# Kernel tuning notes

Measured on AMD Instinct MI355X. Metric: run time of the kernel, lower is better.

Reference implementation:

```python
import jax, jax.numpy as jnp
import numpy as np

NUM_FREQS = 10
Z_SIZE = 256
HIDDEN = 256
N_LAYERS = 8
N_POLY = 100000
PE_DIM = 2 * NUM_FREQS + 2 * NUM_FREQS * 2 + 4  # 64
IN1 = PE_DIM + Z_SIZE        # 320
IN_MID = HIDDEN + IN1        # 576
SLOPE = 0.01


def setup_inputs() -> dict:
    key = jax.random.key(0)
    ks = jax.random.split(key, 12)
    B = 131072
    xy = jax.random.normal(ks[0], (B, 2), dtype=jnp.float32)
    idx = jax.random.randint(ks[1], (B,), 0, N_POLY, dtype=jnp.int64 if jax.config.jax_enable_x64 else jnp.int32)
    emb = jax.random.normal(ks[2], (N_POLY, Z_SIZE), dtype=jnp.float32) * 0.01
    s = 0.02
    W1a = jax.random.normal(ks[3], (IN1, HIDDEN), dtype=jnp.float32) * s
    b1a = jnp.zeros((HIDDEN,), jnp.float32)
    W1b = jax.random.normal(ks[4], (HIDDEN, HIDDEN), dtype=jnp.float32) * s
    b1b = jnp.zeros((HIDDEN,), jnp.float32)
    Wa = jax.random.normal(ks[5], (N_LAYERS, IN_MID, HIDDEN), dtype=jnp.float32) * s
    ba = jnp.zeros((N_LAYERS, HIDDEN), jnp.float32)
    Wb = jax.random.normal(ks[6], (N_LAYERS, HIDDEN, HIDDEN), dtype=jnp.float32) * s
    bb = jnp.zeros((N_LAYERS, HIDDEN), jnp.float32)
    W2 = jax.random.normal(ks[7], (HIDDEN, 1), dtype=jnp.float32) * s
    b2 = jnp.zeros((1,), jnp.float32)
    return {"xy": xy, "idx": idx, "emb": emb, "W1a": W1a, "b1a": b1a,
            "W1b": W1b, "b1b": b1b, "Wa": Wa, "ba": ba, "Wb": Wb, "bb": bb,
            "W2": W2, "b2": b2}


def _pos_encode(xy):
    # linspace freq bands (log_sampling=False default)
    freq = jnp.linspace(1.0, 6.0, NUM_FREQS).astype(xy.dtype)  # (F,)
    xf = xy[:, None, :] * freq[:, None]                         # (B,F,2)
    # cat([x_input, sin, cos], dim=1) then reshape -> (B, (1+2F)*2)
    out = jnp.concatenate([xy[:, None, :], jnp.sin(xf), jnp.cos(xf)], axis=1)
    out = out.reshape(xy.shape[0], -1)                          # (B,42)
    # polar fourier encoding
    r = jnp.sqrt(xy[:, 0] ** 2 + xy[:, 1] ** 2)                 # (B,)
    rf = r[:, None] * freq                                      # (B,F)
    pe = jnp.concatenate([xy, jnp.sin(rf), jnp.cos(rf)], axis=-1)  # (B,22)
    return jnp.concatenate([out, pe], axis=-1)                  # (B,64)


def reference(xy, idx, emb, W1a, b1a, W1b, b1b, Wa, ba, Wb, bb, W2, b2):
    feat = _pos_encode(xy)                       # (B,64)
    z = emb[idx]                                 # (B,256)
    xy_z = jnp.concatenate([feat, z], axis=1)    # (B,320)
    x = jax.nn.leaky_relu(xy_z @ W1a + b1a, SLOPE) @ W1b + b1b  # (B,256)
    for i in range(N_LAYERS):
        h = jnp.concatenate([xy_z, x], axis=1)   # (B,576)
        x = jax.nn.leaky_relu(h @ Wa[i] + ba[i], SLOPE) @ Wb[i] + bb[i]
    return x @ W2 + b2                           # (B,1)
```

## Files before the change

### kernel.cpp

```cpp
#include <hip/hip_runtime.h>
#include <hip/hip_bf16.h>


typedef __attribute__((ext_vector_type(8))) __bf16 bfv8;
typedef __attribute__((ext_vector_type(8))) short s16x8;
typedef __attribute__((ext_vector_type(4))) float f32x4;
typedef __attribute__((ext_vector_type(4))) int i32x4;

__device__ __forceinline__ short f2bf(float f) {
  unsigned u = __builtin_bit_cast(unsigned, f);
  u = (u + 0x7fffu + ((u >> 16) & 1u)) >> 16;
  return (short)u;
}
__device__ __forceinline__ float bf2f(short s) {
  unsigned u = ((unsigned)(unsigned short)s) << 16;
  return __builtin_bit_cast(float, u);
}
__device__ __forceinline__ int swzaddr(int base, int stride, int row, int colbyte) {
  return base + row * stride + (colbyte ^ (((row & 7) << 4) ^ ((row & 8) << 2)));
}
__device__ __forceinline__ void ldsbar() {
  __builtin_amdgcn_sched_barrier(0);
  asm volatile("s_waitcnt lgkmcnt(0)");
  __builtin_amdgcn_s_barrier();
  __builtin_amdgcn_sched_barrier(0);
}

__global__ void pack_weights_kernel(const float* __restrict__ W1a, const float* __restrict__ W1b,
                                    const float* __restrict__ Wa, const float* __restrict__ Wb,
                                    short* __restrict__ ws) {
  int p = blockIdx.x * blockDim.x + threadIdx.x;
  const int P1 = 10240;
  const int P2 = P1 + 8192;
  const int P3 = P2 + 8 * 18432;
  const int P4 = P3 + 8 * 8192;
  if (p >= P4) return;
  const float* src;
  int q;
  if (p < P1)      { src = W1a; q = p; }
  else if (p < P2) { src = W1b; q = p - P1; }
  else if (p < P3) { q = p - P2; int l = q / 18432; q -= l * 18432; src = Wa + l * 147456; }
  else             { q = p - P3; int l = q / 8192;  q -= l * 8192;  src = Wb + l * 65536; }
  const int lane = q & 63, t = q >> 6, nt = t & 15, kt = t >> 4;
  const int k0 = kt * 32 + ((lane >> 4) << 3);
  const int n  = ((nt >> 1) << 5) + ((lane & 15) << 1) + (nt & 1);
  short* dst = ws + (size_t)p * 8;
#pragma unroll
  for (int i = 0; i < 8; ++i) dst[i] = f2bf(src[(size_t)(k0 + i) * 256 + n]);
}

struct BPre { bfv8 b0, b1; };
struct AFrag { bfv8 r0, r1, r2, r3; };
struct Pre { BPre b; AFrag a; };

__device__ __forceinline__ bfv8 bfrag(const short* __restrict__ wp, int kt, int nt, int lane) {
  const short* base = wp + (((size_t)(kt * 16 + nt)) << 9);
  return *(const bfv8*)(base + (lane << 3));
}

template<int NKT, int SPLITKT, bool LEAKY, bool MIDBAR, bool PRE_A, bool PRE_NEXT_A>
__device__ __forceinline__ Pre do_gemm(short* lds,
    int a1Base, int a1S, int a2Base, int a2S,
    const short* __restrict__ wp, const short* __restrict__ wpn,
    const float* __restrict__ bias, int outBase,
    int wc, int lane, Pre pre)
{
  const int lo = lane & 15, hi = lane >> 4;
  const int ntb = wc << 1;
  const float2 bv = *(const float2*)(bias + (wc << 5) + (lo << 1));
  f32x4 acc[4][2];
#pragma unroll
  for (int r = 0; r < 4; ++r) { acc[r][0] = (f32x4)0.f; acc[r][1] = (f32x4)0.f; }

  const int xr  = ((lo & 7) << 4) ^ ((lo & 8) << 2);
  const int hib = hi << 4;
  const char* A1E = (const char*)lds + a1Base + lo * a1S + ((     hib) ^ xr);
  const char* A1O = (const char*)lds + a1Base + lo * a1S + ((64 + hib) ^ xr);
  const char* A2E = (const char*)lds + a2Base + lo * a2S + ((     hib) ^ xr);
  const char* A2O = (const char*)lds + a2Base + lo * a2S + ((64 + hib) ^ xr);

  auto aLoad = [&](int kt, AFrag& dst) {
    const bool g1 = kt < SPLITKT;
    const int kk  = g1 ? kt : kt - SPLITKT;
    const int st  = g1 ? a1S : a2S;
    const char* b = (g1 ? ((kk & 1) ? A1O : A1E) : ((kk & 1) ? A2O : A2E)) + (kk >> 1) * 128;
    dst.r0 = *(const bfv8*)(b);
    dst.r1 = *(const bfv8*)(b + (st << 4));
    dst.r2 = *(const bfv8*)(b + (st << 5));
    dst.r3 = *(const bfv8*)(b + (st << 4) * 3);
  };

  bfv8 bst[4][2];
  AFrag ast[3];
  bst[0][0] = pre.b.b0; bst[0][1] = pre.b.b1;
  if (NKT > 1) { bst[1][0] = bfrag(wp, 1, ntb, lane); bst[1][1] = bfrag(wp, 1, ntb + 1, lane); }
  if (NKT > 2) { bst[2][0] = bfrag(wp, 2, ntb, lane); bst[2][1] = bfrag(wp, 2, ntb + 1, lane); }
  if (PRE_A) ast[0] = pre.a; else aLoad(0, ast[0]);
  if (NKT > 1) aLoad(1, ast[1]);
  Pre nxt;

#pragma unroll
  for (int i = 0; i < NKT; ++i) {
    if (MIDBAR && i == SPLITKT - 2) ldsbar();
    if (i + 3 < NKT) {
      bst[(i + 3) & 3][0] = bfrag(wp, i + 3, ntb, lane);
      bst[(i + 3) & 3][1] = bfrag(wp, i + 3, ntb + 1, lane);
    } else if (i + 3 == NKT || (NKT <= 3 && i == 0)) {
      nxt.b.b0 = bfrag(wpn, 0, ntb, lane);
      nxt.b.b1 = bfrag(wpn, 0, ntb + 1, lane);
    }
    if (i + 2 < NKT) aLoad(i + 2, ast[(i + 2) % 3]);
    if (PRE_NEXT_A && i == NKT - 1) {
      const char* bx = (const char*)lds + lo * 640 + (hib ^ xr);
      nxt.a.r0 = *(const bfv8*)(bx);
      nxt.a.r1 = *(const bfv8*)(bx + 640 * 16);
      nxt.a.r2 = *(const bfv8*)(bx + 640 * 32);
      nxt.a.r3 = *(const bfv8*)(bx + 640 * 48);
    }
    const AFrag& ac = ast[i % 3];
    __builtin_amdgcn_s_setprio(1);
    acc[0][0] = __builtin_amdgcn_mfma_f32_16x16x32_bf16(ac.r0, bst[i & 3][0], acc[0][0], 0, 0, 0);
    acc[0][1] = __builtin_amdgcn_mfma_f32_16x16x32_bf16(ac.r0, bst[i & 3][1], acc[0][1], 0, 0, 0);
    acc[1][0] = __builtin_amdgcn_mfma_f32_16x16x32_bf16(ac.r1, bst[i & 3][0], acc[1][0], 0, 0, 0);
    acc[1][1] = __builtin_amdgcn_mfma_f32_16x16x32_bf16(ac.r1, bst[i & 3][1], acc[1][1], 0, 0, 0);
    acc[2][0] = __builtin_amdgcn_mfma_f32_16x16x32_bf16(ac.r2, bst[i & 3][0], acc[2][0], 0, 0, 0);
    acc[2][1] = __builtin_amdgcn_mfma_f32_16x16x32_bf16(ac.r2, bst[i & 3][1], acc[2][1], 0, 0, 0);
    acc[3][0] = __builtin_amdgcn_mfma_f32_16x16x32_bf16(ac.r3, bst[i & 3][0], acc[3][0], 0, 0, 0);
    acc[3][1] = __builtin_amdgcn_mfma_f32_16x16x32_bf16(ac.r3, bst[i & 3][1], acc[3][1], 0, 0, 0);
    __builtin_amdgcn_s_setprio(0);
  }
#pragma unroll
  for (int rt = 0; rt < 4; ++rt)
#pragma unroll
    for (int rr = 0; rr < 4; ++rr) {
      float v0 = acc[rt][0][rr] + bv.x;
      float v1 = acc[rt][1][rr] + bv.y;
      if (LEAKY) { v0 = fmaxf(v0, 0.01f * v0); v1 = fmaxf(v1, 0.01f * v1); }
      unsigned pk;
      asm("v_cvt_pk_bf16_f32 %0, %1, %2" : "=v"(pk) : "v"(v0), "v"(v1));
      const int orow = (rt << 4) + (hi << 2) + rr;
      *(unsigned*)((char*)lds + swzaddr(outBase, 512, orow, (wc << 6) + (lo << 2))) = pk;
    }
  return nxt;
}

__launch_bounds__(512, 1)
__global__ void geo2vec_kernel(const float* __restrict__ xy, const int* __restrict__ idx,
    const float* __restrict__ emb,
    const float* __restrict__ b1a, const float* __restrict__ b1b,
    const float* __restrict__ ba, const float* __restrict__ bb,
    const float* __restrict__ W2, const float* __restrict__ b2,
    const short* __restrict__ wp, float* __restrict__ out)
{
  __shared__ short lds[53248];
  const int tid = threadIdx.x;
  const int lane = tid & 63;
  const int wc = __builtin_amdgcn_readfirstlane(tid >> 6);

  Pre pre;
  pre.b.b0 = bfrag(wp, 0, (wc << 1), lane);
  pre.b.b1 = bfrag(wp, 0, (wc << 1) + 1, lane);

  {
    const int g = tid >> 3, j = tid & 7;
    const int row = blockIdx.x * 64 + g;
    const float xv = xy[2 * row], yv = xy[2 * row + 1];
    const float rv = sqrtf(xv * xv + yv * yv);
    union { short s[8]; i32x4 v; } tmp;
#pragma unroll
    for (int i = 0; i < 8; ++i) {
      const int c = 8 * j + i;
      float fv;
      if (c < 2)       fv = c ? yv : xv;
      else if (c < 22) { int m = c - 2;  float f = 1.0f + (5.0f / 9.0f) * (m >> 1); fv = sinf(((m & 1) ? yv : xv) * f); }
      else if (c < 42) { int m = c - 22; float f = 1.0f + (5.0f / 9.0f) * (m >> 1); fv = cosf(((m & 1) ? yv : xv) * f); }
      else if (c < 44) fv = (c == 42) ? xv : yv;
      else if (c < 54) fv = sinf(rv * (1.0f + (5.0f / 9.0f) * (c - 44)));
      else             fv = cosf(rv * (1.0f + (5.0f / 9.0f) * (c - 54)));
      tmp.s[i] = f2bf(fv);
    }
    *(i32x4*)((char*)lds + swzaddr(0, 640, g, j << 4)) = tmp.v;
    const float* zr = emb + (size_t)(unsigned)idx[row] * 256;
#pragma unroll
    for (int c4 = 0; c4 < 4; ++c4) {
      const int cel = j * 32 + c4 * 8;
      const float4 f0 = *(const float4*)(zr + cel);
      const float4 f1 = *(const float4*)(zr + cel + 4);
      union { short s[8]; i32x4 v; } t2;
      t2.s[0] = f2bf(f0.x); t2.s[1] = f2bf(f0.y); t2.s[2] = f2bf(f0.z); t2.s[3] = f2bf(f0.w);
      t2.s[4] = f2bf(f1.x); t2.s[5] = f2bf(f1.y); t2.s[6] = f2bf(f1.z); t2.s[7] = f2bf(f1.w);
      *(i32x4*)((char*)lds + swzaddr(0, 640, g, (64 + cel) << 1)) = t2.v;
    }
  }
  ldsbar();

  pre = do_gemm<10, 10, true,  false, false, false>(lds, 0, 640, 0, 640,
        wp, wp + 81920, b1a, 73728, wc, lane, pre);
  ldsbar();
  pre = do_gemm<8, 8, false, false, false, true>(lds, 73728, 512, 73728, 512,
        wp + 81920, wp + 147456, b1b, 40960, wc, lane, pre);
  for (int l = 0; l < 8; ++l) {
    const short* wa = wp + 147456 + l * 147456;
    const short* wb = wp + 1327104 + l * 65536;
    const short* wan = (l < 7) ? (wa + 147456) : wp;
    pre = do_gemm<18, 10, true, true, true, false>(lds, 0, 640, 40960, 512,
          wa, wb, ba + l * 256, 73728, wc, lane, pre);
    ldsbar();
    pre = do_gemm<8, 8, false, false, false, true>(lds, 73728, 512, 73728, 512,
          wb, wan, bb + l * 256, 40960, wc, lane, pre);
  }
  ldsbar();

  {
    const int r = tid >> 3, j = tid & 7;
    float sum = 0.f;
#pragma unroll
    for (int h = 0; h < 4; ++h) {
      const int cb = 64 * j + 16 * h;
      const s16x8 v = *(const s16x8*)((const char*)lds + swzaddr(40960, 512, r, cb));
      const int c0 = 32 * j + 8 * h;
      const float4 w0 = *(const float4*)(W2 + c0);
      const float4 w1 = *(const float4*)(W2 + c0 + 4);
      sum += bf2f(v[0]) * w0.x + bf2f(v[1]) * w0.y + bf2f(v[2]) * w0.z + bf2f(v[3]) * w0.w;
      sum += bf2f(v[4]) * w1.x + bf2f(v[5]) * w1.y + bf2f(v[6]) * w1.z + bf2f(v[7]) * w1.w;
    }
    sum += __shfl_xor(sum, 1); sum += __shfl_xor(sum, 2); sum += __shfl_xor(sum, 4);
    if (j == 0) out[blockIdx.x * 64 + r] = sum + b2[0];
  }
}

extern "C" void kernel_launch(void* const* d_in, const int* in_sizes, int n_in,
                              void* d_out, int out_size, void* d_ws, size_t ws_size,
                              hipStream_t stream) {
  const float* xy  = (const float*)d_in[0];
  const int*   idx = (const int*)d_in[1];
  const float* emb = (const float*)d_in[2];
  const float* W1a = (const float*)d_in[3];
  const float* b1a = (const float*)d_in[4];
  const float* W1b = (const float*)d_in[5];
  const float* b1b = (const float*)d_in[6];
  const float* Wa  = (const float*)d_in[7];
  const float* ba  = (const float*)d_in[8];
  const float* Wb  = (const float*)d_in[9];
  const float* bb  = (const float*)d_in[10];
  const float* W2  = (const float*)d_in[11];
  const float* b2  = (const float*)d_in[12];
  short* ws = (short*)d_ws;
  const int B = in_sizes[1];

  hipLaunchKernelGGL(pack_weights_kernel, dim3(904), dim3(256), 0, stream,
                     W1a, W1b, Wa, Wb, ws);
  hipLaunchKernelGGL(geo2vec_kernel, dim3(B / 64), dim3(512), 0, stream,
                     xy, idx, emb, b1a, b1b, ba, bb, W2, b2, ws, (float*)d_out);
}
```

Baseline: 472.5 us.

## Shrink row tile to 48 per block to fit two blocks per CU

Cuts the rows handled per block from 64 to 48 by dropping one 16-row MFMA tile, and repacks the LDS buffers so shared memory falls from about 106 KB to about 80 KB. The goal is to fit two resident blocks per CU so one block's MFMA work can overlap another's barriers and LDS traffic. Launch bounds are raised to ask for four blocks per CU. A tail guard clamps out-of-range rows. In exchange, each weight fragment loaded from global memory is reused over fewer rows, and the tighter register budget implied by the launch bounds may force spills.

Result: no change. 481.9 us (+2.0%).

```diff
diff --git a/kernel.cpp b/kernel.cpp
--- a/kernel.cpp
+++ b/kernel.cpp
@@ -49,8 +49,11 @@
   for (int i = 0; i < 8; ++i) dst[i] = f2bf(src[(size_t)(k0 + i) * 256 + n]);
 }
 
+#define XB 30720
+#define TB 55296
+
 struct BPre { bfv8 b0, b1; };
-struct AFrag { bfv8 r0, r1, r2, r3; };
+struct AFrag { bfv8 r0, r1, r2; };
 struct Pre { BPre b; AFrag a; };
 
 __device__ __forceinline__ bfv8 bfrag(const short* __restrict__ wp, int kt, int nt, int lane) {
@@ -68,9 +71,9 @@
   const int lo = lane & 15, hi = lane >> 4;
   const int ntb = wc << 1;
   const float2 bv = *(const float2*)(bias + (wc << 5) + (lo << 1));
-  f32x4 acc[4][2];
-#pragma unroll
-  for (int r = 0; r < 4; ++r) { acc[r][0] = (f32x4)0.f; acc[r][1] = (f32x4)0.f; }
+  f32x4 acc[3][2];
+#pragma unroll
+  for (int r = 0; r < 3; ++r) { acc[r][0] = (f32x4)0.f; acc[r][1] = (f32x4)0.f; }
 
   const int xr  = ((lo & 7) << 4) ^ ((lo & 8) << 2);
   const int hib = hi << 4;
@@ -87,7 +90,6 @@
     dst.r0 = *(const bfv8*)(b);
     dst.r1 = *(const bfv8*)(b + (st << 4));
     dst.r2 = *(const bfv8*)(b + (st << 5));
-    dst.r3 = *(const bfv8*)(b + (st << 4) * 3);
   };
 
   bfv8 bst[4][2];
@@ -115,7 +117,6 @@
       nxt.a.r0 = *(const bfv8*)(bx);
       nxt.a.r1 = *(const bfv8*)(bx + 640 * 16);
       nxt.a.r2 = *(const bfv8*)(bx + 640 * 32);
-      nxt.a.r3 = *(const bfv8*)(bx + 640 * 48);
     }
     const AFrag& ac = ast[i % 3];
     __builtin_amdgcn_s_setprio(1);
@@ -125,12 +126,10 @@
     acc[1][1] = __builtin_amdgcn_mfma_f32_16x16x32_bf16(ac.r1, bst[i & 3][1], acc[1][1], 0, 0, 0);
     acc[2][0] = __builtin_amdgcn_mfma_f32_16x16x32_bf16(ac.r2, bst[i & 3][0], acc[2][0], 0, 0, 0);
     acc[2][1] = __builtin_amdgcn_mfma_f32_16x16x32_bf16(ac.r2, bst[i & 3][1], acc[2][1], 0, 0, 0);
-    acc[3][0] = __builtin_amdgcn_mfma_f32_16x16x32_bf16(ac.r3, bst[i & 3][0], acc[3][0], 0, 0, 0);
-    acc[3][1] = __builtin_amdgcn_mfma_f32_16x16x32_bf16(ac.r3, bst[i & 3][1], acc[3][1], 0, 0, 0);
     __builtin_amdgcn_s_setprio(0);
   }
 #pragma unroll
-  for (int rt = 0; rt < 4; ++rt)
+  for (int rt = 0; rt < 3; ++rt)
 #pragma unroll
     for (int rr = 0; rr < 4; ++rr) {
       float v0 = acc[rt][0][rr] + bv.x;
@@ -144,15 +143,15 @@
   return nxt;
 }
 
-__launch_bounds__(512, 1)
+__launch_bounds__(512, 4)
 __global__ void geo2vec_kernel(const float* __restrict__ xy, const int* __restrict__ idx,
     const float* __restrict__ emb,
     const float* __restrict__ b1a, const float* __restrict__ b1b,
     const float* __restrict__ ba, const float* __restrict__ bb,
     const float* __restrict__ W2, const float* __restrict__ b2,
-    const short* __restrict__ wp, float* __restrict__ out)
+    const short* __restrict__ wp, float* __restrict__ out, int Btot)
 {
-  __shared__ short lds[53248];
+  __shared__ short lds[39936];
   const int tid = threadIdx.x;
   const int lane = tid & 63;
   const int wc = __builtin_amdgcn_readfirstlane(tid >> 6);
@@ -163,69 +162,75 @@
 
   {
     const int g = tid >> 3, j = tid & 7;
-    const int row = blockIdx.x * 64 + g;
-    const float xv = xy[2 * row], yv = xy[2 * row + 1];
-    const float rv = sqrtf(xv * xv + yv * yv);
-    union { short s[8]; i32x4 v; } tmp;
-#pragma unroll
-    for (int i = 0; i < 8; ++i) {
-      const int c = 8 * j + i;
-      float fv;
-      if (c < 2)       fv = c ? yv : xv;
-      else if (c < 22) { int m = c - 2;  float f = 1.0f + (5.0f / 9.0f) * (m >> 1); fv = sinf(((m & 1) ? yv : xv) * f); }
-      else if (c < 42) { int m = c - 22; float f = 1.0f + (5.0f / 9.0f) * (m >> 1); fv = cosf(((m & 1) ? yv : xv) * f); }
-      else if (c < 44) fv = (c == 42) ? xv : yv;
-      else if (c < 54) fv = sinf(rv * (1.0f + (5.0f / 9.0f) * (c - 44)));
-      else             fv = cosf(rv * (1.0f + (5.0f / 9.0f) * (c - 54)));
-      tmp.s[i] = f2bf(fv);
-    }
-    *(i32x4*)((char*)lds + swzaddr(0, 640, g, j << 4)) = tmp.v;
-    const float* zr = emb + (size_t)(unsigned)idx[row] * 256;
-#pragma unroll
-    for (int c4 = 0; c4 < 4; ++c4) {
-      const int cel = j * 32 + c4 * 8;
-      const float4 f0 = *(const float4*)(zr + cel);
-      const float4 f1 = *(const float4*)(zr + cel + 4);
-      union { short s[8]; i32x4 v; } t2;
-      t2.s[0] = f2bf(f0.x); t2.s[1] = f2bf(f0.y); t2.s[2] = f2bf(f0.z); t2.s[3] = f2bf(f0.w);
-      t2.s[4] = f2bf(f1.x); t2.s[5] = f2bf(f1.y); t2.s[6] = f2bf(f1.z); t2.s[7] = f2bf(f1.w);
-      *(i32x4*)((char*)lds + swzaddr(0, 640, g, (64 + cel) << 1)) = t2.v;
+    if (g < 48) {
+      int grow = blockIdx.x * 48 + g;
+      if (grow >= Btot) grow = Btot - 1;
+      const float xv = xy[2 * grow], yv = xy[2 * grow + 1];
+      const float rv = sqrtf(xv * xv + yv * yv);
+      union { short s[8]; i32x4 v; } tmp;
+#pragma unroll
+      for (int i = 0; i < 8; ++i) {
+        const int c = 8 * j + i;
+        float fv;
+        if (c < 2)       fv = c ? yv : xv;
+        else if (c < 22) { int m = c - 2;  float f = 1.0f + (5.0f / 9.0f) * (m >> 1); fv = sinf(((m & 1) ? yv : xv) * f); }
+        else if (c < 42) { int m = c - 22; float f = 1.0f + (5.0f / 9.0f) * (m >> 1); fv = cosf(((m & 1) ? yv : xv) * f); }
+        else if (c < 44) fv = (c == 42) ? xv : yv;
+        else if (c < 54) fv = sinf(rv * (1.0f + (5.0f / 9.0f) * (c - 44)));
+        else             fv = cosf(rv * (1.0f + (5.0f / 9.0f) * (c - 54)));
+        tmp.s[i] = f2bf(fv);
+      }
+      *(i32x4*)((char*)lds + swzaddr(0, 640, g, j << 4)) = tmp.v;
+      const float* zr = emb + (size_t)(unsigned)idx[grow] * 256;
+#pragma unroll
+      for (int c4 = 0; c4 < 4; ++c4) {
+        const int cel = j * 32 + c4 * 8;
+        const float4 f0 = *(const float4*)(zr + cel);
+        const float4 f1 = *(const float4*)(zr + cel + 4);
+        union { short s[8]; i32x4 v; } t2;
+        t2.s[0] = f2bf(f0.x); t2.s[1] = f2bf(f0.y); t2.s[2] = f2bf(f0.z); t2.s[3] = f2bf(f0.w);
+        t2.s[4] = f2bf(f1.x); t2.s[5] = f2bf(f1.y); t2.s[6] = f2bf(f1.z); t2.s[7] = f2bf(f1.w);
+        *(i32x4*)((char*)lds + swzaddr(0, 640, g, (64 + cel) << 1)) = t2.v;
+      }
     }
   }
   ldsbar();
 
   pre = do_gemm<10, 10, true,  false, false, false>(lds, 0, 640, 0, 640,
-        wp, wp + 81920, b1a, 73728, wc, lane, pre);
+        wp, wp + 81920, b1a, TB, wc, lane, pre);
   ldsbar();
-  pre = do_gemm<8, 8, false, false, false, true>(lds, 73728, 512, 73728, 512,
-        wp + 81920, wp + 147456, b1b, 40960, wc, lane, pre);
+  pre = do_gemm<8, 8, false, false, false, true>(lds, TB, 512, TB, 512,
+        wp + 81920, wp + 147456, b1b, XB, wc, lane, pre);
   for (int l = 0; l < 8; ++l) {
     const short* wa = wp + 147456 + l * 147456;
     const short* wb = wp + 1327104 + l * 65536;
     const short* wan = (l < 7) ? (wa + 147456) : wp;
-    pre = do_gemm<18, 10, true, true, true, false>(lds, 0, 640, 40960, 512,
-          wa, wb, ba + l * 256, 73728, wc, lane, pre);
+    pre = do_gemm<18, 10, true, true, true, false>(lds, 0, 640, XB, 512,
+          wa, wb, ba + l * 256, TB, wc, lane, pre);
     ldsbar();
-    pre = do_gemm<8, 8, false, false, false, true>(lds, 73728, 512, 73728, 512,
-          wb, wan, bb + l * 256, 40960, wc, lane, pre);
+    pre = do_gemm<8, 8, false, false, false, true>(lds, TB, 512, TB, 512,
+          wb, wan, bb + l * 256, XB, wc, lane, pre);
   }
   ldsbar();
 
   {
     const int r = tid >> 3, j = tid & 7;
-    float sum = 0.f;
-#pragma unroll
-    for (int h = 0; h < 4; ++h) {
-      const int cb = 64 * j + 16 * h;
-      const s16x8 v = *(const s16x8*)((const char*)lds + swzaddr(40960, 512, r, cb));
-      const int c0 = 32 * j + 8 * h;
-      const float4 w0 = *(const float4*)(W2 + c0);
-      const float4 w1 = *(const float4*)(W2 + c0 + 4);
-      sum += bf2f(v[0]) * w0.x + bf2f(v[1]) * w0.y + bf2f(v[2]) * w0.z + bf2f(v[3]) * w0.w;
-      sum += bf2f(v[4]) * w1.x + bf2f(v[5]) * w1.y + bf2f(v[6]) * w1.z + bf2f(v[7]) * w1.w;
-    }
-    sum += __shfl_xor(sum, 1); sum += __shfl_xor(sum, 2); sum += __shfl_xor(sum, 4);
-    if (j == 0) out[blockIdx.x * 64 + r] = sum + b2[0];
+    if (r < 48) {
+      float sum = 0.f;
+#pragma unroll
+      for (int h = 0; h < 4; ++h) {
+        const int cb = 64 * j + 16 * h;
+        const s16x8 v = *(const s16x8*)((const char*)lds + swzaddr(XB, 512, r, cb));
+        const int c0 = 32 * j + 8 * h;
+        const float4 w0 = *(const float4*)(W2 + c0);
+        const float4 w1 = *(const float4*)(W2 + c0 + 4);
+        sum += bf2f(v[0]) * w0.x + bf2f(v[1]) * w0.y + bf2f(v[2]) * w0.z + bf2f(v[3]) * w0.w;
+        sum += bf2f(v[4]) * w1.x + bf2f(v[5]) * w1.y + bf2f(v[6]) * w1.z + bf2f(v[7]) * w1.w;
+      }
+      sum += __shfl_xor(sum, 1); sum += __shfl_xor(sum, 2); sum += __shfl_xor(sum, 4);
+      const int grow = blockIdx.x * 48 + r;
+      if (j == 0 && grow < Btot) out[grow] = sum + b2[0];
+    }
   }
 }
 
@@ -250,6 +255,6 @@
 
   hipLaunchKernelGGL(pack_weights_kernel, dim3(904), dim3(256), 0, stream,
                      W1a, W1b, Wa, Wb, ws);
-  hipLaunchKernelGGL(geo2vec_kernel, dim3(B / 64), dim3(512), 0, stream,
-                     xy, idx, emb, b1a, b1b, ba, bb, W2, b2, ws, (float*)d_out);
-}
+  hipLaunchKernelGGL(geo2vec_kernel, dim3((B + 47) / 48), dim3(512), 0, stream,
+                     xy, idx, emb, b1a, b1b, ba, bb, W2, b2, ws, (float*)d_out, B);
+}
```

## Switch GEMMs from 16x16x32 to 32x32x16 bf16 MFMA tiles

Applied to the files above, without the earlier changes.

Replaces the 16x16x32 MFMA tiling with 32x32x16 MFMA instructions. The weight packing layout, fragment loads, A-operand LDS addressing, pipelining depth and epilogue store pattern all change to match. Each wave now issues fewer, larger MFMAs per k-step and loads half as many A fragments, which should raise operand reuse. In exchange the epilogue writes individual 16-bit values to LDS instead of packed pairs, and two alternating accumulators are kept to hide MFMA dependency latency.

Result: slower. 568.6 us (+20.3%).

```diff
diff --git a/kernel.cpp b/kernel.cpp
--- a/kernel.cpp
+++ b/kernel.cpp
@@ -4,7 +4,7 @@
 
 typedef __attribute__((ext_vector_type(8))) __bf16 bfv8;
 typedef __attribute__((ext_vector_type(8))) short s16x8;
-typedef __attribute__((ext_vector_type(4))) float f32x4;
+typedef __attribute__((ext_vector_type(16))) float f32x16;
 typedef __attribute__((ext_vector_type(4))) int i32x4;
 
 __device__ __forceinline__ short f2bf(float f) {
@@ -41,106 +41,96 @@
   else if (p < P2) { src = W1b; q = p - P1; }
   else if (p < P3) { q = p - P2; int l = q / 18432; q -= l * 18432; src = Wa + l * 147456; }
   else             { q = p - P3; int l = q / 8192;  q -= l * 8192;  src = Wb + l * 65536; }
-  const int lane = q & 63, t = q >> 6, nt = t & 15, kt = t >> 4;
-  const int k0 = kt * 32 + ((lane >> 4) << 3);
-  const int n  = ((nt >> 1) << 5) + ((lane & 15) << 1) + (nt & 1);
+  const int lane = q & 63, t = q >> 6, nt = t & 7, kt = t >> 3;
+  const int k0 = (kt << 4) + ((lane >> 5) << 3);
+  const int n  = (nt << 5) + (lane & 31);
   short* dst = ws + (size_t)p * 8;
 #pragma unroll
   for (int i = 0; i < 8; ++i) dst[i] = f2bf(src[(size_t)(k0 + i) * 256 + n]);
 }
 
-struct BPre { bfv8 b0, b1; };
-struct AFrag { bfv8 r0, r1, r2, r3; };
-struct Pre { BPre b; AFrag a; };
-
-__device__ __forceinline__ bfv8 bfrag(const short* __restrict__ wp, int kt, int nt, int lane) {
-  const short* base = wp + (((size_t)(kt * 16 + nt)) << 9);
+#define XB 40960
+#define TB 73728
+
+struct AF { bfv8 r0, r1; };
+struct Pre { bfv8 b; AF a; };
+
+__device__ __forceinline__ bfv8 bfrag(const short* __restrict__ wp, int kt16, int nt32, int lane) {
+  const short* base = wp + (((size_t)((kt16 << 3) + nt32)) << 9);
   return *(const bfv8*)(base + (lane << 3));
 }
 
-template<int NKT, int SPLITKT, bool LEAKY, bool MIDBAR, bool PRE_A, bool PRE_NEXT_A>
+template<int NKT, int SPLIT, bool LEAKY, bool MIDBAR, bool PRE_A, bool PRE_NEXT_A>
 __device__ __forceinline__ Pre do_gemm(short* lds,
     int a1Base, int a1S, int a2Base, int a2S,
     const short* __restrict__ wp, const short* __restrict__ wpn,
     const float* __restrict__ bias, int outBase,
     int wc, int lane, Pre pre)
 {
-  const int lo = lane & 15, hi = lane >> 4;
-  const int ntb = wc << 1;
-  const float2 bv = *(const float2*)(bias + (wc << 5) + (lo << 1));
-  f32x4 acc[4][2];
-#pragma unroll
-  for (int r = 0; r < 4; ++r) { acc[r][0] = (f32x4)0.f; acc[r][1] = (f32x4)0.f; }
-
-  const int xr  = ((lo & 7) << 4) ^ ((lo & 8) << 2);
-  const int hib = hi << 4;
-  const char* A1E = (const char*)lds + a1Base + lo * a1S + ((     hib) ^ xr);
-  const char* A1O = (const char*)lds + a1Base + lo * a1S + ((64 + hib) ^ xr);
-  const char* A2E = (const char*)lds + a2Base + lo * a2S + ((     hib) ^ xr);
-  const char* A2O = (const char*)lds + a2Base + lo * a2S + ((64 + hib) ^ xr);
-
-  auto aLoad = [&](int kt, AFrag& dst) {
-    const bool g1 = kt < SPLITKT;
-    const int kk  = g1 ? kt : kt - SPLITKT;
+  const int row = lane & 31;
+  const int xr  = ((row & 7) << 4) ^ ((row & 8) << 2);
+  const int kl  = (lane >> 5) << 4;
+  const float bv = bias[(wc << 5) + row];
+
+  f32x16 acc[2][2];
+#pragma unroll
+  for (int r = 0; r < 2; ++r) { acc[r][0] = (f32x16)0.f; acc[r][1] = (f32x16)0.f; }
+
+  const char* A1[4]; const char* A2[4];
+#pragma unroll
+  for (int m = 0; m < 4; ++m) {
+    A1[m] = (const char*)lds + a1Base + row * a1S + (((m << 5) + kl) ^ xr);
+    A2[m] = (const char*)lds + a2Base + row * a2S + (((m << 5) + kl) ^ xr);
+  }
+  auto aLoad = [&](int kt, AF& dst) {
+    const bool g1 = kt < SPLIT;
+    const int kk  = g1 ? kt : kt - SPLIT;
     const int st  = g1 ? a1S : a2S;
-    const char* b = (g1 ? ((kk & 1) ? A1O : A1E) : ((kk & 1) ? A2O : A2E)) + (kk >> 1) * 128;
+    const char* b = (g1 ? A1[kk & 3] : A2[kk & 3]) + (kk >> 2) * 128;
     dst.r0 = *(const bfv8*)(b);
-    dst.r1 = *(const bfv8*)(b + (st << 4));
-    dst.r2 = *(const bfv8*)(b + (st << 5));
-    dst.r3 = *(const bfv8*)(b + (st << 4) * 3);
+    dst.r1 = *(const bfv8*)(b + (st << 5));
   };
 
-  bfv8 bst[4][2];
-  AFrag ast[3];
-  bst[0][0] = pre.b.b0; bst[0][1] = pre.b.b1;
-  if (NKT > 1) { bst[1][0] = bfrag(wp, 1, ntb, lane); bst[1][1] = bfrag(wp, 1, ntb + 1, lane); }
-  if (NKT > 2) { bst[2][0] = bfrag(wp, 2, ntb, lane); bst[2][1] = bfrag(wp, 2, ntb + 1, lane); }
+  bfv8 bst[4];
+  AF ast[2];
+  bst[0] = pre.b;
+  if (NKT > 1) bst[1] = bfrag(wp, 1, wc, lane);
+  if (NKT > 2) bst[2] = bfrag(wp, 2, wc, lane);
   if (PRE_A) ast[0] = pre.a; else aLoad(0, ast[0]);
-  if (NKT > 1) aLoad(1, ast[1]);
   Pre nxt;
 
 #pragma unroll
   for (int i = 0; i < NKT; ++i) {
-    if (MIDBAR && i == SPLITKT - 2) ldsbar();
+    if (MIDBAR && i == SPLIT - 2) ldsbar();
     if (i + 3 < NKT) {
-      bst[(i + 3) & 3][0] = bfrag(wp, i + 3, ntb, lane);
-      bst[(i + 3) & 3][1] = bfrag(wp, i + 3, ntb + 1, lane);
+      bst[(i + 3) & 3] = bfrag(wp, i + 3, wc, lane);
     } else if (i + 3 == NKT || (NKT <= 3 && i == 0)) {
-      nxt.b.b0 = bfrag(wpn, 0, ntb, lane);
-      nxt.b.b1 = bfrag(wpn, 0, ntb + 1, lane);
-    }
-    if (i + 2 < NKT) aLoad(i + 2, ast[(i + 2) % 3]);
+      nxt.b = bfrag(wpn, 0, wc, lane);
+    }
+    if (i + 1 < NKT) aLoad(i + 1, ast[(i + 1) & 1]);
     if (PRE_NEXT_A && i == NKT - 1) {
-      const char* bx = (const char*)lds + lo * 640 + (hib ^ xr);
+      const char* bx = (const char*)lds + row * 640 + (kl ^ xr);
       nxt.a.r0 = *(const bfv8*)(bx);
-      nxt.a.r1 = *(const bfv8*)(bx + 640 * 16);
-      nxt.a.r2 = *(const bfv8*)(bx + 640 * 32);
-      nxt.a.r3 = *(const bfv8*)(bx + 640 * 48);
-    }
-    const AFrag& ac = ast[i % 3];
+      nxt.a.r1 = *(const bfv8*)(bx + (640 << 5));
+    }
+    const AF& ac = ast[i & 1];
     __builtin_amdgcn_s_setprio(1);
-    acc[0][0] = __builtin_amdgcn_mfma_f32_16x16x32_bf16(ac.r0, bst[i & 3][0], acc[0][0], 0, 0, 0);
-    acc[0][1] = __builtin_amdgcn_mfma_f32_16x16x32_bf16(ac.r0, bst[i & 3][1], acc[0][1], 0, 0, 0);
-    acc[1][0] = __builtin_amdgcn_mfma_f32_16x16x32_bf16(ac.r1, bst[i & 3][0], acc[1][0], 0, 0, 0);
-    acc[1][1] = __builtin_amdgcn_mfma_f32_16x16x32_bf16(ac.r1, bst[i & 3][1], acc[1][1], 0, 0, 0);
-    acc[2][0] = __builtin_amdgcn_mfma_f32_16x16x32_bf16(ac.r2, bst[i & 3][0], acc[2][0], 0, 0, 0);
-    acc[2][1] = __builtin_amdgcn_mfma_f32_16x16x32_bf16(ac.r2, bst[i & 3][1], acc[2][1], 0, 0, 0);
-    acc[3][0] = __builtin_amdgcn_mfma_f32_16x16x32_bf16(ac.r3, bst[i & 3][0], acc[3][0], 0, 0, 0);
-    acc[3][1] = __builtin_amdgcn_mfma_f32_16x16x32_bf16(ac.r3, bst[i & 3][1], acc[3][1], 0, 0, 0);
+    acc[0][i & 1] = __builtin_amdgcn_mfma_f32_32x32x16_bf16(ac.r0, bst[i & 3], acc[0][i & 1], 0, 0, 0);
+    acc[1][i & 1] = __builtin_amdgcn_mfma_f32_32x32x16_bf16(ac.r1, bst[i & 3], acc[1][i & 1], 0, 0, 0);
     __builtin_amdgcn_s_setprio(0);
   }
-#pragma unroll
-  for (int rt = 0; rt < 4; ++rt)
-#pragma unroll
-    for (int rr = 0; rr < 4; ++rr) {
-      float v0 = acc[rt][0][rr] + bv.x;
-      float v1 = acc[rt][1][rr] + bv.y;
-      if (LEAKY) { v0 = fmaxf(v0, 0.01f * v0); v1 = fmaxf(v1, 0.01f * v1); }
-      unsigned pk;
-      asm("v_cvt_pk_bf16_f32 %0, %1, %2" : "=v"(pk) : "v"(v0), "v"(v1));
-      const int orow = (rt << 4) + (hi << 2) + rr;
-      *(unsigned*)((char*)lds + swzaddr(outBase, 512, orow, (wc << 6) + (lo << 2))) = pk;
-    }
+  const int colb = ((wc << 5) + row) << 1;
+#pragma unroll
+  for (int rt = 0; rt < 2; ++rt) {
+    const f32x16 a = acc[rt][0] + acc[rt][1];
+#pragma unroll
+    for (int r = 0; r < 16; ++r) {
+      float v = a[r] + bv;
+      if (LEAKY) v = fmaxf(v, 0.01f * v);
+      const int orow = (rt << 5) + (r & 3) + ((r >> 2) << 3) + ((lane >> 5) << 2);
+      *(short*)((char*)lds + swzaddr(outBase, 512, orow, colb)) = f2bf(v);
+    }
+  }
   return nxt;
 }
 
@@ -158,8 +148,7 @@
   const int wc = __builtin_amdgcn_readfirstlane(tid >> 6);
 
   Pre pre;
-  pre.b.b0 = bfrag(wp, 0, (wc << 1), lane);
-  pre.b.b1 = bfrag(wp, 0, (wc << 1) + 1, lane);
+  pre.b = bfrag(wp, 0, wc, lane);
 
   {
     const int g = tid >> 3, j = tid & 7;
@@ -194,20 +183,20 @@
   }
   ldsbar();
 
-  pre = do_gemm<10, 10, true,  false, false, false>(lds, 0, 640, 0, 640,
-        wp, wp + 81920, b1a, 73728, wc, lane, pre);
+  pre = do_gemm<20, 20, true,  false, false, false>(lds, 0, 640, 0, 640,
+        wp, wp + 81920, b1a, TB, wc, lane, pre);
   ldsbar();
-  pre = do_gemm<8, 8, false, false, false, true>(lds, 73728, 512, 73728, 512,
-        wp + 81920, wp + 147456, b1b, 40960, wc, lane, pre);
+  pre = do_gemm<16, 16, false, false, false, true>(lds, TB, 512, TB, 512,
+        wp + 81920, wp + 147456, b1b, XB, wc, lane, pre);
   for (int l = 0; l < 8; ++l) {
     const short* wa = wp + 147456 + l * 147456;
     const short* wb = wp + 1327104 + l * 65536;
     const short* wan = (l < 7) ? (wa + 147456) : wp;
-    pre = do_gemm<18, 10, true, true, true, false>(lds, 0, 640, 40960, 512,
-          wa, wb, ba + l * 256, 73728, wc, lane, pre);
+    pre = do_gemm<36, 20, true, true, true, false>(lds, 0, 640, XB, 512,
+          wa, wb, ba + l * 256, TB, wc, lane, pre);
     ldsbar();
-    pre = do_gemm<8, 8, false, false, false, true>(lds, 73728, 512, 73728, 512,
-          wb, wan, bb + l * 256, 40960, wc, lane, pre);
+    pre = do_gemm<16, 16, false, false, false, true>(lds, TB, 512, TB, 512,
+          wb, wan, bb + l * 256, XB, wc, lane, pre);
   }
   ldsbar();
 
@@ -217,7 +206,7 @@
 #pragma unroll
     for (int h = 0; h < 4; ++h) {
       const int cb = 64 * j + 16 * h;
-      const s16x8 v = *(const s16x8*)((const char*)lds + swzaddr(40960, 512, r, cb));
+      const s16x8 v = *(const s16x8*)((const char*)lds + swzaddr(XB, 512, r, cb));
       const int c0 = 32 * j + 8 * h;
       const float4 w0 = *(const float4*)(W2 + c0);
       const float4 w1 = *(const float4*)(W2 + c0 + 4);
```
